# Kernel tuning notes

Hardware: AMD Instinct MI355X
Metric: run time of the kernel (lower is better)

## Reference

```python
import jax, jax.numpy as jnp
import numpy as np

N_NEURONS = 2048
IN_DIM = 1024
OUT_DIM = 1024
TOKENS = 4096
TIME_STEPS = 3
DENSITY = 0.25


def setup_inputs() -> dict:
    key = jax.random.key(0)
    ks = jax.random.split(key, 10)
    x = jax.random.normal(ks[0], (TOKENS, IN_DIM), dtype=jnp.float32)
    W_in = jax.random.normal(ks[1], (N_NEURONS, IN_DIM), dtype=jnp.float32) * (1.0 / np.sqrt(IN_DIM))
    b_in = jax.random.normal(ks[2], (N_NEURONS,), dtype=jnp.float32) * 0.01
    weights = jax.random.normal(ks[3], (N_NEURONS, N_NEURONS), dtype=jnp.float32) * 0.3
    J = jax.random.normal(ks[4], (N_NEURONS, N_NEURONS), dtype=jnp.float32) * 0.1
    theta = jax.random.uniform(ks[5], (N_NEURONS,), dtype=jnp.float32) * 1.0 + 0.25
    lam = jnp.asarray(0.35, dtype=jnp.float32)
    # connection mask: rand < density, zero diagonal (buffer, fixed)
    m = (jax.random.uniform(ks[6], (N_NEURONS, N_NEURONS)) < DENSITY).astype(jnp.float32)
    mask = m * (1.0 - jnp.eye(N_NEURONS, dtype=jnp.float32))
    noise_raw = jax.random.normal(ks[7], (TIME_STEPS, TOKENS, N_NEURONS), dtype=jnp.float32)
    W_out = jax.random.normal(ks[8], (OUT_DIM, N_NEURONS), dtype=jnp.float32) * (1.0 / np.sqrt(N_NEURONS))
    b_out = jax.random.normal(ks[9], (OUT_DIM,), dtype=jnp.float32) * 0.01
    return {"x": x, "W_in": W_in, "b_in": b_in, "weights": weights, "J": J,
            "theta": theta, "lam": lam, "mask": mask, "noise_raw": noise_raw,
            "W_out": W_out, "b_out": b_out, "time_steps": TIME_STEPS}


def reference(x, W_in, b_in, weights, J, theta, lam, mask, noise_raw, W_out, b_out, time_steps):
    # input projection: [tokens, in_dim] -> [tokens, n]
    state = x @ W_in.T + b_in
    eff_w = weights * mask          # [n, n]
    J_m = J * mask                  # [n, n]
    T = jnp.abs(jnp.sin(2.0 * theta))  # temperature [n]
    for t in range(time_steps):
        signal = state @ eff_w                     # [tokens, n]
        s = jnp.tanh(state)
        # einsum('bi,ij,bj->bj', s, J_m, s) == (s @ J_m) * s
        delta = (s @ J_m) * s                      # [tokens, n]
        noise = noise_raw[t] * T * 0.1             # [tokens, n]
        state = jnp.tanh(signal + lam * delta + noise)
    return state @ W_out.T + b_out
```

## Files before the change

kernel.cpp:

```cpp
#include <hip/hip_runtime.h>
#include <hip/hip_fp16.h>

#define TOKENS 4096
#define NN 2048
#define IN_DIM 1024
#define OUT_DIM 1024
#define TSTEPS 3

typedef _Float16 half8 __attribute__((ext_vector_type(8)));
typedef _Float16 half4 __attribute__((ext_vector_type(4)));
typedef float f32x4 __attribute__((ext_vector_type(4)));

__device__ __forceinline__ void gload_lds16(const void* g, void* l) {
    __builtin_amdgcn_global_load_lds(
        (const __attribute__((address_space(1))) unsigned*)g,
        (__attribute__((address_space(3))) unsigned*)l, 16, 0, 0);
}

#define LGKM(N) asm volatile("s_waitcnt lgkmcnt(" #N ")" ::: "memory")
#define VMCNT(N) asm volatile("s_waitcnt vmcnt(" #N ")" ::: "memory")
#define SCHED0() __builtin_amdgcn_sched_barrier(0)

__global__ __launch_bounds__(512, 2)
void dual_gemm(const _Float16* __restrict__ A0g, const _Float16* __restrict__ B0g,
               float* __restrict__ C0,
               const _Float16* __restrict__ A1g, const _Float16* __restrict__ B1g,
               float* __restrict__ C1)
{
    __shared__ __align__(16) _Float16 lds[2 * 32768];
    const int tid  = threadIdx.x;
    const int wid  = tid >> 6;
    const int lane = tid & 63;

    const int raw  = blockIdx.x;
    const int widx = (raw & 7) * 32 + (raw >> 3);
    const int g    = widx >> 7;
    const int bid  = widx & 127;
    const int by = bid >> 3;
    const int bx = bid & 7;
    const _Float16* __restrict__ A = g ? A1g : A0g;
    const _Float16* __restrict__ B = g ? B1g : B0g;
    float* __restrict__ C = g ? C1 : C0;
    const int brow = by << 8;
    const int bcol = bx << 8;

    const int sr = tid >> 3;
    const int sc = ((tid & 7) ^ (sr & 7)) << 3;
    const _Float16* gA = A + (size_t)(brow + sr) * NN + sc;
    const _Float16* gB = B + (size_t)(bcol + sr) * NN + sc;
    const int ldst = wid << 9;

    auto stA = [&](int T, int h) {
        _Float16* l = lds + (T & 1) * 32768 + h * 8192;
        const _Float16* p = gA + (size_t)(h << 7) * NN + (T << 6);
        gload_lds16(p,           l + ldst);
        gload_lds16(p + 64 * NN, l + 4096 + ldst);
    };
    auto stB = [&](int T, int h) {
        _Float16* l = lds + (T & 1) * 32768 + 16384 + h * 8192;
        const _Float16* p = gB + (size_t)(h << 7) * NN + (T << 6);
        gload_lds16(p,           l + ldst);
        gload_lds16(p + 64 * NN, l + 4096 + ldst);
    };

    const int wr = (wid >> 2) << 7;
    const int wc = (wid & 3) << 6;
    const int lr = lane & 15;
    const int lq = lane >> 4;
    const int x7 = lr & 7;
    const int c0 = (lq ^ x7) << 3;
    const int c1 = ((4 + lq) ^ x7) << 3;
    const int aRow = (wr + lr) << 6;
    const int bRow = 16384 + ((wc + lr) << 6);

    f32x4 acc[8][4];
#pragma unroll
    for (int m = 0; m < 8; ++m)
#pragma unroll
        for (int n = 0; n < 4; ++n) acc[m][n] = (f32x4){0.f, 0.f, 0.f, 0.f};

    half8 af0[4], af1[4], af2[4], af3[4], bf0[4], bf1[4];

    stA(0, 0); stA(0, 1); stB(0, 0); stB(0, 1);
    stA(1, 0); stA(1, 1); stB(1, 0); stB(1, 1);
    VMCNT(8);
    __builtin_amdgcn_s_barrier();
    {
        const _Float16* lb = lds;
#pragma unroll
        for (int m = 0; m < 4; ++m) af0[m] = *(const half8*)&lb[aRow + (m << 10) + c0];
#pragma unroll
        for (int n = 0; n < 4; ++n) bf0[n] = *(const half8*)&lb[bRow + (n << 10) + c0];
    }

    for (int T = 0; T < 32; ++T) {
        const _Float16* lb = lds + (T & 1) * 32768;

#pragma unroll
        for (int m = 0; m < 4; ++m) af1[m] = *(const half8*)&lb[aRow + ((m + 4) << 10) + c0];
        LGKM(4);
        SCHED0();
        __builtin_amdgcn_s_setprio(1);
#pragma unroll
        for (int m = 0; m < 4; ++m)
#pragma unroll
            for (int n = 0; n < 4; ++n)
                acc[m][n] = __builtin_amdgcn_mfma_f32_16x16x32_f16(af0[m], bf0[n], acc[m][n], 0, 0, 0);
        __builtin_amdgcn_s_setprio(0);
        SCHED0();

#pragma unroll
        for (int m = 0; m < 4; ++m) af2[m] = *(const half8*)&lb[aRow + (m << 10) + c1];
#pragma unroll
        for (int n = 0; n < 4; ++n) bf1[n] = *(const half8*)&lb[bRow + (n << 10) + c1];
        LGKM(8);
        SCHED0();
        __builtin_amdgcn_s_setprio(1);
#pragma unroll
        for (int m = 0; m < 4; ++m)
#pragma unroll
            for (int n = 0; n < 4; ++n)
                acc[m + 4][n] = __builtin_amdgcn_mfma_f32_16x16x32_f16(af1[m], bf0[n], acc[m + 4][n], 0, 0, 0);
        __builtin_amdgcn_s_setprio(0);
        SCHED0();

#pragma unroll
        for (int m = 0; m < 4; ++m) af3[m] = *(const half8*)&lb[aRow + ((m + 4) << 10) + c1];
        LGKM(4);
        SCHED0();
        __builtin_amdgcn_s_setprio(1);
#pragma unroll
        for (int m = 0; m < 4; ++m)
#pragma unroll
            for (int n = 0; n < 4; ++n)
                acc[m][n] = __builtin_amdgcn_mfma_f32_16x16x32_f16(af2[m], bf1[n], acc[m][n], 0, 0, 0);
        __builtin_amdgcn_s_setprio(0);
        SCHED0();

        LGKM(0);
        __builtin_amdgcn_s_barrier();
        if (T < 30) { stA(T + 2, 0); stA(T + 2, 1); stB(T + 2, 0); stB(T + 2, 1); }
        if (T < 30) { VMCNT(8); }
        else        { VMCNT(0); }
        __builtin_amdgcn_s_barrier();
        asm volatile("" ::: "memory");

        if (T < 31) {
            const _Float16* ln = lds + ((T + 1) & 1) * 32768;
#pragma unroll
            for (int m = 0; m < 4; ++m) af0[m] = *(const half8*)&ln[aRow + (m << 10) + c0];
#pragma unroll
            for (int n = 0; n < 4; ++n) bf0[n] = *(const half8*)&ln[bRow + (n << 10) + c0];
        }
        SCHED0();
        __builtin_amdgcn_s_setprio(1);
#pragma unroll
        for (int m = 0; m < 4; ++m)
#pragma unroll
            for (int n = 0; n < 4; ++n)
                acc[m + 4][n] = __builtin_amdgcn_mfma_f32_16x16x32_f16(af3[m], bf1[n], acc[m + 4][n], 0, 0, 0);
        __builtin_amdgcn_s_setprio(0);
        SCHED0();
    }

    const int cr = lq << 2;
    const int cc = lane & 15;
#pragma unroll
    for (int m = 0; m < 8; ++m) {
#pragma unroll
        for (int n = 0; n < 4; ++n) {
            const size_t o0 = (size_t)(brow + wr + m * 16 + cr) * NN
                            + (bcol + wc + n * 16 + cc);
#pragma unroll
            for (int j = 0; j < 4; ++j)
                C[o0 + (size_t)j * NN] = acc[m][n][j];
        }
    }
}

template<int EPI>
__global__ __launch_bounds__(256)
void gemm_bt(const _Float16* __restrict__ A, const _Float16* __restrict__ B,
             float* __restrict__ C, const float* __restrict__ bias,
             _Float16* __restrict__ oSta, _Float16* __restrict__ oS,
             int M, int N, int K)
{
    __shared__ _Float16 As[128 * 32];
    __shared__ _Float16 Bs[128 * 32];
    const int tid  = threadIdx.x;
    const int wid  = tid >> 6;
    const int lane = tid & 63;
    const int wr = (wid >> 1) * 64;
    const int wc = (wid & 1) * 64;
    const int brow = blockIdx.y * 128;
    const int bcol = blockIdx.x * 128;

    f32x4 acc[4][4];
#pragma unroll
    for (int m = 0; m < 4; ++m)
#pragma unroll
        for (int n = 0; n < 4; ++n) acc[m][n] = (f32x4){0.f, 0.f, 0.f, 0.f};

    const int ldr = tid >> 2;
    const int ldc = (tid & 3) * 8;
    const int wbase = (wid << 4) * 32;
    const int kq = (lane >> 4) * 8;
    const int lr = lane & 15;

    for (int k0 = 0; k0 < K; k0 += 32) {
        __syncthreads();
        gload_lds16(A + (size_t)(brow + ldr) * K + k0 + ldc, As + wbase);
        gload_lds16(A + (size_t)(brow + 64 + ldr) * K + k0 + ldc, As + 64 * 32 + wbase);
        gload_lds16(B + (size_t)(bcol + ldr) * K + k0 + ldc, Bs + wbase);
        gload_lds16(B + (size_t)(bcol + 64 + ldr) * K + k0 + ldc, Bs + 64 * 32 + wbase);
        __syncthreads();

        half8 af[4], bf[4];
#pragma unroll
        for (int m = 0; m < 4; ++m)
            af[m] = *(const half8*)&As[(wr + m * 16 + lr) * 32 + kq];
#pragma unroll
        for (int n = 0; n < 4; ++n)
            bf[n] = *(const half8*)&Bs[(wc + n * 16 + lr) * 32 + kq];
#pragma unroll
        for (int m = 0; m < 4; ++m)
#pragma unroll
            for (int n = 0; n < 4; ++n)
                acc[m][n] = __builtin_amdgcn_mfma_f32_16x16x32_f16(af[m], bf[n], acc[m][n], 0, 0, 0);
    }

    const int cr = (lane >> 4) * 4;
    const int cc = lane & 15;
#pragma unroll
    for (int m = 0; m < 4; ++m) {
#pragma unroll
        for (int n = 0; n < 4; ++n) {
            const int ccol = bcol + wc + n * 16 + cc;
#pragma unroll
            for (int j = 0; j < 4; ++j) {
                const int crow = brow + wr + m * 16 + cr + j;
                float v = acc[m][n][j];
                const size_t o = (size_t)crow * N + ccol;
                if (EPI == 1) {
                    v += bias[ccol];
                    oSta[o] = (_Float16)v;
                    oS[o] = (_Float16)tanhf(v);
                } else {
                    C[o] = v + bias[ccol];
                }
            }
        }
    }
}

__global__ void cvt_f16(const float* __restrict__ in, _Float16* __restrict__ out, int n4) {
    int i = blockIdx.x * blockDim.x + threadIdx.x;
    if (i < n4) {
        f32x4 v = *(const f32x4*)&in[(size_t)i * 4];
        half4 h;
        h[0] = (_Float16)v[0]; h[1] = (_Float16)v[1];
        h[2] = (_Float16)v[2]; h[3] = (_Float16)v[3];
        *(half4*)&out[(size_t)i * 4] = h;
    }
}

__global__ void transmul2(const float* __restrict__ W, const float* __restrict__ J,
                          const float* __restrict__ Mk,
                          _Float16* __restrict__ effT, _Float16* __restrict__ JmT) {
    __shared__ float tw[32][33];
    __shared__ float tj[32][33];
    const int bx = blockIdx.x * 32, by = blockIdx.y * 32;
    const int tx = threadIdx.x, ty0 = threadIdx.y;
#pragma unroll
    for (int r = 0; r < 4; ++r) {
        int ty = ty0 + r * 8;
        size_t idx = (size_t)(by + ty) * NN + bx + tx;
        float mv = Mk[idx];
        tw[ty][tx] = W[idx] * mv;
        tj[ty][tx] = J[idx] * mv;
    }
    __syncthreads();
#pragma unroll
    for (int r = 0; r < 4; ++r) {
        int ty = ty0 + r * 8;
        size_t o = (size_t)(bx + ty) * NN + by + tx;
        effT[o] = (_Float16)tw[tx][ty];
        JmT[o]  = (_Float16)tj[tx][ty];
    }
}

__global__ void tsc_kernel(const float* __restrict__ theta, float* __restrict__ Tsc) {
    int i = blockIdx.x * blockDim.x + threadIdx.x;
    if (i < NN) Tsc[i] = fabsf(sinf(2.0f * theta[i])) * 0.1f;
}

__global__ void step_kernel(const float* __restrict__ signal, const float* __restrict__ sJ,
                            const float* __restrict__ noise, const float* __restrict__ Tsc,
                            const float* __restrict__ lamp,
                            _Float16* __restrict__ stateH, _Float16* __restrict__ sH) {
    const int i4 = blockIdx.x * blockDim.x + threadIdx.x;
    const float lam = lamp[0];
    const size_t base = (size_t)i4 * 4;
    f32x4 sg = *(const f32x4*)&signal[base];
    f32x4 dj = *(const f32x4*)&sJ[base];
    f32x4 nz = *(const f32x4*)&noise[base];
    const int col4 = (int)(base & (NN - 1));
    f32x4 tv = *(const f32x4*)&Tsc[col4];
    half4 so = *(const half4*)&sH[base];
    half4 hs, hn;
#pragma unroll
    for (int j = 0; j < 4; ++j) {
        float s = (float)so[j];
        float arg = sg[j] + lam * (dj[j] * s) + nz[j] * tv[j];
        float st = tanhf(arg);
        hs[j] = (_Float16)st;
        hn[j] = (_Float16)tanhf(st);
    }
    *(half4*)&stateH[base] = hs;
    *(half4*)&sH[base] = hn;
}

extern "C" void kernel_launch(void* const* d_in, const int* in_sizes, int n_in,
                              void* d_out, int out_size, void* d_ws, size_t ws_size,
                              hipStream_t stream) {
    const float* x       = (const float*)d_in[0];
    const float* W_in    = (const float*)d_in[1];
    const float* b_in    = (const float*)d_in[2];
    const float* weights = (const float*)d_in[3];
    const float* Jmat    = (const float*)d_in[4];
    const float* theta   = (const float*)d_in[5];
    const float* lam     = (const float*)d_in[6];
    const float* mask    = (const float*)d_in[7];
    const float* noise   = (const float*)d_in[8];
    const float* W_out   = (const float*)d_in[9];
    const float* b_out   = (const float*)d_in[10];
    float* out = (float*)d_out;

    char* w = (char*)d_ws;
    auto alloc = [&](size_t b) { char* p = w; w += (b + 255) & ~(size_t)255; return p; };
    _Float16* xh     = (_Float16*)alloc((size_t)TOKENS * IN_DIM * 2);
    _Float16* WinH   = (_Float16*)alloc((size_t)NN * IN_DIM * 2);
    _Float16* WoutH  = (_Float16*)alloc((size_t)OUT_DIM * NN * 2);
    _Float16* effT   = (_Float16*)alloc((size_t)NN * NN * 2);
    _Float16* JmT    = (_Float16*)alloc((size_t)NN * NN * 2);
    _Float16* stateH = (_Float16*)alloc((size_t)TOKENS * NN * 2);
    _Float16* sH     = (_Float16*)alloc((size_t)TOKENS * NN * 2);
    float* Tsc       = (float*)alloc((size_t)NN * 4);
    float* signal    = (float*)alloc((size_t)TOKENS * NN * 4);
    float* sJ        = (float*)alloc((size_t)TOKENS * NN * 4);

    cvt_f16<<<TOKENS * IN_DIM / 4 / 256, 256, 0, stream>>>(x, xh, TOKENS * IN_DIM / 4);
    cvt_f16<<<NN * IN_DIM / 4 / 256, 256, 0, stream>>>(W_in, WinH, NN * IN_DIM / 4);
    cvt_f16<<<OUT_DIM * NN / 4 / 256, 256, 0, stream>>>(W_out, WoutH, OUT_DIM * NN / 4);
    transmul2<<<dim3(NN / 32, NN / 32), dim3(32, 8), 0, stream>>>(weights, Jmat, mask, effT, JmT);
    tsc_kernel<<<NN / 256, 256, 0, stream>>>(theta, Tsc);

    gemm_bt<1><<<dim3(NN / 128, TOKENS / 128), 256, 0, stream>>>(
        xh, WinH, nullptr, b_in, stateH, sH, TOKENS, NN, IN_DIM);

    for (int t = 0; t < TSTEPS; ++t) {
        dual_gemm<<<256, 512, 0, stream>>>(stateH, effT, signal, sH, JmT, sJ);
        step_kernel<<<TOKENS * NN / 4 / 256, 256, 0, stream>>>(
            signal, sJ, noise + (size_t)t * TOKENS * NN, Tsc, lam, stateH, sH);
    }

    gemm_bt<2><<<dim3(OUT_DIM / 128, TOKENS / 128), 256, 0, stream>>>(
        stateH, WoutH, out, b_out, nullptr, nullptr, TOKENS, OUT_DIM, NN);
}
```

Before: 370.4 us.

## Pipeline input/output GEMMs and store dual-GEMM intermediates in fp16

Replaces the simple single-buffered input and output projection GEMM with a double-buffered, LDS-swizzled, software-pipelined kernel that uses a 64-wide K tile, grouped block ordering and prioritized MFMA issue. The dual GEMM now writes signal and s@J_m as fp16 instead of fp32, and the step kernel reads them as fp16. This halves the intermediate write and read traffic each time step. The cost is reduced precision of the pre-activation terms.

After: 341.1 us. 7.9% less time.

```diff
diff --git a/kernel.cpp b/kernel.cpp
--- a/kernel.cpp
+++ b/kernel.cpp
@@ -23,9 +23,9 @@
 
 __global__ __launch_bounds__(512, 2)
 void dual_gemm(const _Float16* __restrict__ A0g, const _Float16* __restrict__ B0g,
-               float* __restrict__ C0,
+               _Float16* __restrict__ C0,
                const _Float16* __restrict__ A1g, const _Float16* __restrict__ B1g,
-               float* __restrict__ C1)
+               _Float16* __restrict__ C1)
 {
     __shared__ __align__(16) _Float16 lds[2 * 32768];
     const int tid  = threadIdx.x;
@@ -40,7 +40,7 @@
     const int bx = bid & 7;
     const _Float16* __restrict__ A = g ? A1g : A0g;
     const _Float16* __restrict__ B = g ? B1g : B0g;
-    float* __restrict__ C = g ? C1 : C0;
+    _Float16* __restrict__ C = g ? C1 : C0;
     const int brow = by << 8;
     const int bcol = bx << 8;
 
@@ -173,27 +173,61 @@
                             + (bcol + wc + n * 16 + cc);
 #pragma unroll
             for (int j = 0; j < 4; ++j)
-                C[o0 + (size_t)j * NN] = acc[m][n][j];
+                C[o0 + (size_t)j * NN] = (_Float16)acc[m][n][j];
         }
     }
 }
 
 template<int EPI>
-__global__ __launch_bounds__(256)
-void gemm_bt(const _Float16* __restrict__ A, const _Float16* __restrict__ B,
-             float* __restrict__ C, const float* __restrict__ bias,
-             _Float16* __restrict__ oSta, _Float16* __restrict__ oS,
-             int M, int N, int K)
+__global__ __launch_bounds__(256, 2)
+void pgemm(const _Float16* __restrict__ A, const _Float16* __restrict__ B,
+           float* __restrict__ Cout, const float* __restrict__ bias,
+           _Float16* __restrict__ oSta, _Float16* __restrict__ oS,
+           int K, int N, int nbxLog2)
 {
-    __shared__ _Float16 As[128 * 32];
-    __shared__ _Float16 Bs[128 * 32];
+    __shared__ __align__(16) _Float16 lds[2 * 16384];
     const int tid  = threadIdx.x;
     const int wid  = tid >> 6;
     const int lane = tid & 63;
-    const int wr = (wid >> 1) * 64;
-    const int wc = (wid & 1) * 64;
-    const int brow = blockIdx.y * 128;
-    const int bcol = blockIdx.x * 128;
+
+    const int raw  = blockIdx.x;
+    const int cpx  = gridDim.x >> 3;
+    const int widx = (raw & 7) * cpx + (raw >> 3);
+    const int by = widx >> nbxLog2;
+    const int bx = widx & ((1 << nbxLog2) - 1);
+    const int brow = by << 7;
+    const int bcol = bx << 7;
+
+    const int sr = tid >> 3;
+    const int sc = ((tid & 7) ^ (sr & 7)) << 3;
+    const _Float16* gA = A + (size_t)(brow + sr) * K + sc;
+    const _Float16* gB = B + (size_t)(bcol + sr) * K + sc;
+    const int ldst = wid << 9;
+
+    auto stA = [&](int T) {
+        _Float16* l = lds + (T & 1) * 16384;
+        const _Float16* p = gA + (T << 6);
+#pragma unroll
+        for (int r = 0; r < 4; ++r)
+            gload_lds16(p + (size_t)(r * 32) * K, l + r * 2048 + ldst);
+    };
+    auto stB = [&](int T) {
+        _Float16* l = lds + (T & 1) * 16384 + 8192;
+        const _Float16* p = gB + (T << 6);
+#pragma unroll
+        for (int r = 0; r < 4; ++r)
+            gload_lds16(p + (size_t)(r * 32) * K, l + r * 2048 + ldst);
+    };
+
+    const int wr = (wid >> 1) << 6;
+    const int wc = (wid & 1) << 6;
+    const int lr = lane & 15;
+    const int lq = lane >> 4;
+    const int x7 = lr & 7;
+    const int c0 = (lq ^ x7) << 3;
+    const int c1 = ((4 + lq) ^ x7) << 3;
+    const int aRow = (wr + lr) << 6;
+    const int bRow = 8192 + ((wc + lr) << 6);
 
     f32x4 acc[4][4];
 #pragma unroll
@@ -201,35 +235,64 @@
 #pragma unroll
         for (int n = 0; n < 4; ++n) acc[m][n] = (f32x4){0.f, 0.f, 0.f, 0.f};
 
-    const int ldr = tid >> 2;
-    const int ldc = (tid & 3) * 8;
-    const int wbase = (wid << 4) * 32;
-    const int kq = (lane >> 4) * 8;
-    const int lr = lane & 15;
-
-    for (int k0 = 0; k0 < K; k0 += 32) {
-        __syncthreads();
-        gload_lds16(A + (size_t)(brow + ldr) * K + k0 + ldc, As + wbase);
-        gload_lds16(A + (size_t)(brow + 64 + ldr) * K + k0 + ldc, As + 64 * 32 + wbase);
-        gload_lds16(B + (size_t)(bcol + ldr) * K + k0 + ldc, Bs + wbase);
-        gload_lds16(B + (size_t)(bcol + 64 + ldr) * K + k0 + ldc, Bs + 64 * 32 + wbase);
-        __syncthreads();
-
-        half8 af[4], bf[4];
-#pragma unroll
-        for (int m = 0; m < 4; ++m)
-            af[m] = *(const half8*)&As[(wr + m * 16 + lr) * 32 + kq];
-#pragma unroll
-        for (int n = 0; n < 4; ++n)
-            bf[n] = *(const half8*)&Bs[(wc + n * 16 + lr) * 32 + kq];
-#pragma unroll
-        for (int m = 0; m < 4; ++m)
-#pragma unroll
-            for (int n = 0; n < 4; ++n)
-                acc[m][n] = __builtin_amdgcn_mfma_f32_16x16x32_f16(af[m], bf[n], acc[m][n], 0, 0, 0);
-    }
-
-    const int cr = (lane >> 4) * 4;
+    half8 af0[4], af1[4], bf0[4], bf1[4];
+    const int NT = K >> 6;
+
+    stA(0); stB(0); stA(1); stB(1);
+    VMCNT(8);
+    __builtin_amdgcn_s_barrier();
+    {
+        const _Float16* lb = lds;
+#pragma unroll
+        for (int m = 0; m < 4; ++m) af0[m] = *(const half8*)&lb[aRow + (m << 10) + c0];
+#pragma unroll
+        for (int n = 0; n < 4; ++n) bf0[n] = *(const half8*)&lb[bRow + (n << 10) + c0];
+    }
+
+    for (int T = 0; T < NT; ++T) {
+        const _Float16* lb = lds + (T & 1) * 16384;
+
+#pragma unroll
+        for (int m = 0; m < 4; ++m) af1[m] = *(const half8*)&lb[aRow + (m << 10) + c1];
+#pragma unroll
+        for (int n = 0; n < 4; ++n) bf1[n] = *(const half8*)&lb[bRow + (n << 10) + c1];
+        LGKM(8);
+        SCHED0();
+        __builtin_amdgcn_s_setprio(1);
+#pragma unroll
+        for (int m = 0; m < 4; ++m)
+#pragma unroll
+            for (int n = 0; n < 4; ++n)
+                acc[m][n] = __builtin_amdgcn_mfma_f32_16x16x32_f16(af0[m], bf0[n], acc[m][n], 0, 0, 0);
+        __builtin_amdgcn_s_setprio(0);
+        SCHED0();
+
+        LGKM(0);
+        __builtin_amdgcn_s_barrier();
+        if (T < NT - 2) { stA(T + 2); stB(T + 2); VMCNT(8); }
+        else if (T == NT - 2) { VMCNT(0); }
+        __builtin_amdgcn_s_barrier();
+        asm volatile("" ::: "memory");
+
+        if (T < NT - 1) {
+            const _Float16* ln = lds + ((T + 1) & 1) * 16384;
+#pragma unroll
+            for (int m = 0; m < 4; ++m) af0[m] = *(const half8*)&ln[aRow + (m << 10) + c0];
+#pragma unroll
+            for (int n = 0; n < 4; ++n) bf0[n] = *(const half8*)&ln[bRow + (n << 10) + c0];
+        }
+        SCHED0();
+        __builtin_amdgcn_s_setprio(1);
+#pragma unroll
+        for (int m = 0; m < 4; ++m)
+#pragma unroll
+            for (int n = 0; n < 4; ++n)
+                acc[m][n] = __builtin_amdgcn_mfma_f32_16x16x32_f16(af1[m], bf1[n], acc[m][n], 0, 0, 0);
+        __builtin_amdgcn_s_setprio(0);
+        SCHED0();
+    }
+
+    const int cr = lq << 2;
     const int cc = lane & 15;
 #pragma unroll
     for (int m = 0; m < 4; ++m) {
@@ -239,14 +302,13 @@
 #pragma unroll
             for (int j = 0; j < 4; ++j) {
                 const int crow = brow + wr + m * 16 + cr + j;
-                float v = acc[m][n][j];
+                float v = acc[m][n][j] + bias[ccol];
                 const size_t o = (size_t)crow * N + ccol;
                 if (EPI == 1) {
-                    v += bias[ccol];
                     oSta[o] = (_Float16)v;
                     oS[o] = (_Float16)tanhf(v);
                 } else {
-                    C[o] = v + bias[ccol];
+                    Cout[o] = v;
                 }
             }
         }
@@ -294,15 +356,15 @@
     if (i < NN) Tsc[i] = fabsf(sinf(2.0f * theta[i])) * 0.1f;
 }
 
-__global__ void step_kernel(const float* __restrict__ signal, const float* __restrict__ sJ,
+__global__ void step_kernel(const _Float16* __restrict__ signalH, const _Float16* __restrict__ sJH,
                             const float* __restrict__ noise, const float* __restrict__ Tsc,
                             const float* __restrict__ lamp,
                             _Float16* __restrict__ stateH, _Float16* __restrict__ sH) {
     const int i4 = blockIdx.x * blockDim.x + threadIdx.x;
     const float lam = lamp[0];
     const size_t base = (size_t)i4 * 4;
-    f32x4 sg = *(const f32x4*)&signal[base];
-    f32x4 dj = *(const f32x4*)&sJ[base];
+    half4 sg = *(const half4*)&signalH[base];
+    half4 dj = *(const half4*)&sJH[base];
     f32x4 nz = *(const f32x4*)&noise[base];
     const int col4 = (int)(base & (NN - 1));
     f32x4 tv = *(const f32x4*)&Tsc[col4];
@@ -311,7 +373,7 @@
 #pragma unroll
     for (int j = 0; j < 4; ++j) {
         float s = (float)so[j];
-        float arg = sg[j] + lam * (dj[j] * s) + nz[j] * tv[j];
+        float arg = (float)sg[j] + lam * ((float)dj[j] * s) + nz[j] * tv[j];
         float st = tanhf(arg);
         hs[j] = (_Float16)st;
         hn[j] = (_Float16)tanhf(st);
@@ -338,16 +400,16 @@
 
     char* w = (char*)d_ws;
     auto alloc = [&](size_t b) { char* p = w; w += (b + 255) & ~(size_t)255; return p; };
-    _Float16* xh     = (_Float16*)alloc((size_t)TOKENS * IN_DIM * 2);
-    _Float16* WinH   = (_Float16*)alloc((size_t)NN * IN_DIM * 2);
-    _Float16* WoutH  = (_Float16*)alloc((size_t)OUT_DIM * NN * 2);
-    _Float16* effT   = (_Float16*)alloc((size_t)NN * NN * 2);
-    _Float16* JmT    = (_Float16*)alloc((size_t)NN * NN * 2);
-    _Float16* stateH = (_Float16*)alloc((size_t)TOKENS * NN * 2);
-    _Float16* sH     = (_Float16*)alloc((size_t)TOKENS * NN * 2);
-    float* Tsc       = (float*)alloc((size_t)NN * 4);
-    float* signal    = (float*)alloc((size_t)TOKENS * NN * 4);
-    float* sJ        = (float*)alloc((size_t)TOKENS * NN * 4);
+    _Float16* xh      = (_Float16*)alloc((size_t)TOKENS * IN_DIM * 2);
+    _Float16* WinH    = (_Float16*)alloc((size_t)NN * IN_DIM * 2);
+    _Float16* WoutH   = (_Float16*)alloc((size_t)OUT_DIM * NN * 2);
+    _Float16* effT    = (_Float16*)alloc((size_t)NN * NN * 2);
+    _Float16* JmT     = (_Float16*)alloc((size_t)NN * NN * 2);
+    _Float16* stateH  = (_Float16*)alloc((size_t)TOKENS * NN * 2);
+    _Float16* sH      = (_Float16*)alloc((size_t)TOKENS * NN * 2);
+    _Float16* signalH = (_Float16*)alloc((size_t)TOKENS * NN * 2);
+    _Float16* sJH     = (_Float16*)alloc((size_t)TOKENS * NN * 2);
+    float* Tsc        = (float*)alloc((size_t)NN * 4);
 
     cvt_f16<<<TOKENS * IN_DIM / 4 / 256, 256, 0, stream>>>(x, xh, TOKENS * IN_DIM / 4);
     cvt_f16<<<NN * IN_DIM / 4 / 256, 256, 0, stream>>>(W_in, WinH, NN * IN_DIM / 4);
@@ -355,15 +417,15 @@
     transmul2<<<dim3(NN / 32, NN / 32), dim3(32, 8), 0, stream>>>(weights, Jmat, mask, effT, JmT);
     tsc_kernel<<<NN / 256, 256, 0, stream>>>(theta, Tsc);
 
-    gemm_bt<1><<<dim3(NN / 128, TOKENS / 128), 256, 0, stream>>>(
-        xh, WinH, nullptr, b_in, stateH, sH, TOKENS, NN, IN_DIM);
+    pgemm<1><<<(TOKENS / 128) * (NN / 128), 256, 0, stream>>>(
+        xh, WinH, nullptr, b_in, stateH, sH, IN_DIM, NN, 4);
 
     for (int t = 0; t < TSTEPS; ++t) {
-        dual_gemm<<<256, 512, 0, stream>>>(stateH, effT, signal, sH, JmT, sJ);
+        dual_gemm<<<256, 512, 0, stream>>>(stateH, effT, signalH, sH, JmT, sJH);
         step_kernel<<<TOKENS * NN / 4 / 256, 256, 0, stream>>>(
-            signal, sJ, noise + (size_t)t * TOKENS * NN, Tsc, lam, stateH, sH);
-    }
-
-    gemm_bt<2><<<dim3(OUT_DIM / 128, TOKENS / 128), 256, 0, stream>>>(
-        stateH, WoutH, out, b_out, nullptr, nullptr, TOKENS, OUT_DIM, NN);
-}
+            signalH, sJH, noise + (size_t)t * TOKENS * NN, Tsc, lam, stateH, sH);
+    }
+
+    pgemm<2><<<(TOKENS / 128) * (OUT_DIM / 128), 256, 0, stream>>>(
+        stateH, WoutH, out, b_out, nullptr, nullptr, NN, OUT_DIM, 3);
+}
```
